# Kernel optimization log

Measured on AMD Instinct MI355X. Metric: run time of the kernel, lower is better.

The kernel has to match this reference:

```python
import jax, jax.numpy as jnp
import numpy as np

NUM_HEADS = 12


def setup_inputs() -> dict:
    key = jax.random.key(0)
    k1, k2, k3 = jax.random.split(key, 3)
    B, N, D = 8, 1024, 768
    x = jax.random.normal(k1, (B, N, D), dtype=jnp.float32)
    Wqkv = jax.random.normal(k2, (D, 3 * D), dtype=jnp.float32) * (D ** -0.5)
    Wproj = jax.random.normal(k3, (D, D), dtype=jnp.float32) * (D ** -0.5)
    bproj = jnp.zeros((D,), dtype=jnp.float32)
    return {"x": x, "Wqkv": Wqkv, "Wproj": Wproj, "bproj": bproj}


def reference(x, Wqkv, Wproj, bproj):
    B, N, D = x.shape
    H = NUM_HEADS
    d = D // H
    scale = d ** -0.5
    qkv = x @ Wqkv  # [B, N, 3D]; qkv_bias=False
    # 'b n (qkv h d) -> qkv b h n d'
    qkv = qkv.reshape(B, N, 3, H, d)
    q = jnp.transpose(qkv[:, :, 0], (0, 2, 1, 3))  # [B, H, N, d]
    k = jnp.transpose(qkv[:, :, 1], (0, 2, 1, 3))
    v = jnp.transpose(qkv[:, :, 2], (0, 2, 1, 3))
    attn = jnp.einsum('bhnd,bhmd->bhnm', q, k) * scale  # [B, H, N, N]
    attn = jax.nn.softmax(attn, axis=-1)
    out = jnp.einsum('bhnm,bhmd->bhnd', attn, v)  # [B, H, N, d]
    out = jnp.transpose(out, (0, 2, 1, 3)).reshape(B, N, D)  # 'b h n d -> b n (h d)'
    return out @ Wproj + bproj
```

## Files before the change

kernel.cpp:

```cpp
#include <hip/hip_runtime.h>
#include <math.h>
#include <stdint.h>

namespace {

constexpr int Nseq = 1024;
constexpr int Dm = 768;
constexpr int threeD = 2304;
constexpr int Mrows = 8192;
constexpr int Hh = 12;
constexpr float kScaleLog2 = 0.18033688011112042f;

using bf16x8 = __attribute__((ext_vector_type(8))) short;
using f32x4 = __attribute__((ext_vector_type(4))) float;
using f32x16 = __attribute__((ext_vector_type(16))) float;
using us4 = __attribute__((ext_vector_type(4))) unsigned short;

__device__ __forceinline__ unsigned short f2bf(float f) {
  union { float f; uint32_t u; } v;
  v.f = f;
  uint32_t r = v.u + 0x7fffu + ((v.u >> 16) & 1u);
  return (unsigned short)(r >> 16);
}

__device__ __forceinline__ float fexp2(float x) {
#if __has_builtin(__builtin_amdgcn_exp2f)
  return __builtin_amdgcn_exp2f(x);
#else
  float r;
  asm("v_exp_f32 %0, %1\n\ts_nop 0" : "=v"(r) : "v"(x));
  return r;
#endif
}

__device__ __forceinline__ uint32_t cvtpk_bf16(float lo, float hi) {
  uint32_t r;
  asm("v_cvt_pk_bf16_f32 %0, %1, %2" : "=v"(r) : "v"(lo), "v"(hi));
  return r;
}

__device__ __forceinline__ void gload_lds16(const void* g, void* l) {
  __builtin_amdgcn_global_load_lds(
      (const __attribute__((address_space(1))) unsigned int*)(uintptr_t)g,
      (__attribute__((address_space(3))) unsigned int*)(uintptr_t)l, 16, 0, 0);
}

__global__ __launch_bounds__(256) void cast_f32_bf16(
    const float* __restrict__ in, unsigned short* __restrict__ outp, int n4) {
  int i = blockIdx.x * blockDim.x + threadIdx.x;
  if (i < n4) {
    float4 v = ((const float4*)in)[i];
    us4 u = {f2bf(v.x), f2bf(v.y), f2bf(v.z), f2bf(v.w)};
    ((us4*)outp)[i] = u;
  }
}

__global__ __launch_bounds__(256) void transpose_cast(
    const float* __restrict__ W, unsigned short* __restrict__ Wt, int K, int N) {
  __shared__ unsigned short tile[32][33];
  const int n0 = blockIdx.x * 32, k0 = blockIdx.y * 32;
  const int tx = threadIdx.x & 31, ty = threadIdx.x >> 5;
#pragma unroll
  for (int i = 0; i < 32; i += 8)
    tile[ty + i][tx] = f2bf(W[(size_t)(k0 + ty + i) * N + n0 + tx]);
  __syncthreads();
#pragma unroll
  for (int i = 0; i < 32; i += 8)
    Wt[(size_t)(n0 + ty + i) * K + k0 + tx] = tile[tx][ty + i];
}

template <int MODE, int BM, int NCOLS>
__global__ __launch_bounds__(256) void gemm_bf16(
    const unsigned short* __restrict__ A, const unsigned short* __restrict__ Bt,
    void* __restrict__ C0, void* __restrict__ C1,
    const float* __restrict__ bias, int K) {
  constexpr int ASL = BM * 4;
  constexpr int TS = ASL + 512;
  constexpr int LPS = TS / 256;
  constexpr int MF = BM / 32;
  __shared__ unsigned short As[3][ASL * 8];
  __shared__ unsigned short Bs[3][512 * 8];
  const int tid = threadIdx.x;
  const int wid = tid >> 6;
  const int lane = tid & 63;
  const int l15 = lane & 15, lg = lane >> 4;
  const int p = blockIdx.x;
  const int cpx = gridDim.x >> 3;
  const int l = (p & 7) * cpx + (p >> 3);
  const int row0 = (l / NCOLS) * BM, col0 = (l % NCOLS) * 128;
  const int wr = (wid >> 1) * (BM / 2), wc = (wid & 1) * 64;

  auto stage = [&](int k0, int bufi) {
    unsigned short* as = As[bufi];
    unsigned short* bs = Bs[bufi];
#pragma unroll
    for (int it = 0; it < LPS; ++it) {
      const int s = it * 256 + tid;
      if (s < ASL) {
        const int r = s >> 2, c = s & 3;
        const int g = c ^ ((r >> 1) & 3);
        gload_lds16(&A[(size_t)(row0 + r) * K + k0 + g * 8],
                    &as[(s & ~63) * 8]);
      } else {
        const int s2 = s - ASL;
        const int r = s2 >> 2, c = s2 & 3;
        const int g = c ^ ((r >> 1) & 3);
        gload_lds16(&Bt[(size_t)(col0 + r) * K + k0 + g * 8],
                    &bs[(s2 & ~63) * 8]);
      }
    }
  };

  f32x4 acc[MF][4] = {};
  const int nt = K / 32;
  stage(0, 0);
  stage(32, 1);
  for (int t = 0; t < nt; ++t) {
    const int cur = t % 3;
    if (t + 2 < nt) {
      stage((t + 2) * 32, (t + 2) % 3);
      asm volatile("s_waitcnt vmcnt(%0)" ::"i"(2 * LPS) : "memory");
    } else if (t + 1 < nt) {
      asm volatile("s_waitcnt vmcnt(%0)" ::"i"(LPS) : "memory");
    } else {
      asm volatile("s_waitcnt vmcnt(0)" ::: "memory");
    }
    __builtin_amdgcn_s_barrier();
    bf16x8 av[MF], bv[4];
#pragma unroll
    for (int m = 0; m < MF; ++m) {
      const int ar = wr + m * 16 + l15;
      av[m] = *(const bf16x8*)&As[cur][(ar * 4 + (lg ^ ((ar >> 1) & 3))) * 8];
    }
#pragma unroll
    for (int n = 0; n < 4; ++n) {
      const int br = wc + n * 16 + l15;
      bv[n] = *(const bf16x8*)&Bs[cur][(br * 4 + (lg ^ ((br >> 1) & 3))) * 8];
    }
#pragma unroll
    for (int m = 0; m < MF; ++m)
#pragma unroll
      for (int n = 0; n < 4; ++n)
        acc[m][n] =
            __builtin_amdgcn_mfma_f32_16x16x32_bf16(av[m], bv[n], acc[m][n], 0, 0, 0);
    asm volatile("s_waitcnt lgkmcnt(0)" ::: "memory");
    __builtin_amdgcn_sched_barrier(0);
    __builtin_amdgcn_s_barrier();
  }
  if constexpr (MODE == 1) {
#pragma unroll
    for (int m = 0; m < MF; ++m)
#pragma unroll
      for (int n = 0; n < 4; ++n) {
        const int col = col0 + wc + n * 16 + l15;
#pragma unroll
        for (int rr = 0; rr < 4; ++rr)
          ((float*)C0)[(size_t)(row0 + wr + m * 16 + lg * 4 + rr) * Dm + col] =
              acc[m][n][rr] + bias[col];
      }
  } else if (col0 < 1536) {
#pragma unroll
    for (int m = 0; m < MF; ++m)
#pragma unroll
      for (int n = 0; n < 4; ++n) {
        const int col = col0 + wc + n * 16 + l15;
        const float qs = (col < 768) ? kScaleLog2 : 1.f;
#pragma unroll
        for (int rr = 0; rr < 4; ++rr)
          ((unsigned short*)C0)[(size_t)(row0 + wr + m * 16 + lg * 4 + rr) * 1536 +
                                col] = f2bf(acc[m][n][rr] * qs);
      }
  } else {
#pragma unroll
    for (int m = 0; m < MF; ++m)
#pragma unroll
      for (int n = 0; n < 4; ++n) {
        const int c = col0 + wc + n * 16 + l15 - 1536;
        const int row = row0 + wr + m * 16 + lg * 4;
        const int bb = row >> 10, n0 = row & 1023;
        us4 pk = {f2bf(acc[m][n][0]), f2bf(acc[m][n][1]), f2bf(acc[m][n][2]),
                  f2bf(acc[m][n][3])};
        *(us4*)&((unsigned short*)C1)[((size_t)bb * 768 + c) * 1024 + n0] = pk;
      }
  }
}

__global__ __launch_bounds__(256) void attn_mfma(
    const unsigned short* __restrict__ qkb, const unsigned short* __restrict__ vtb,
    unsigned short* __restrict__ outb) {
  constexpr int NT = Nseq / 64;
  __shared__ unsigned short Ks[3][64 * 64];
  __shared__ unsigned short Vs[3][64 * 64];
  const int tid = threadIdx.x;
  const int wid = tid >> 6, lane = tid & 63;
  const int l31 = lane & 31, hi = lane >> 5;
  const int p = blockIdx.x;
  const int l = (p & 7) * 96 + (p >> 3);
  const int qt = l & 7;
  const int hb = l >> 3;
  const int h = hb % Hh, b = hb / Hh;
  const size_t rb = (size_t)b * Nseq;
  const int hoff = h * 64;
  const size_t vbase = ((size_t)b * 768 + hoff) * 1024;

  const int qrow = qt * 128 + wid * 32 + l31;
  bf16x8 Qf[4];
#pragma unroll
  for (int ks = 0; ks < 4; ++ks)
    Qf[ks] = *(const bf16x8*)&qkb[(rb + qrow) * 1536 + hoff + ks * 16 + hi * 8];

  int strow[2], scol[2];
#pragma unroll
  for (int it = 0; it < 2; ++it) {
    const int ci = it * 256 + wid * 64 + lane;
    const int tr = ci >> 3, cc = ci & 7;
    strow[it] = tr;
    scol[it] = (cc ^ (tr & 7)) * 8;
  }

  auto stage = [&](int kt, int bufi) {
#pragma unroll
    for (int it = 0; it < 2; ++it) {
      const int ldsoff = (it * 256 + wid * 64) * 8;
      gload_lds16(&qkb[(rb + kt * 64 + strow[it]) * 1536 + 768 + hoff + scol[it]],
                  &Ks[bufi][ldsoff]);
      gload_lds16(&vtb[vbase + (size_t)strow[it] * 1024 + kt * 64 + scol[it]],
                  &Vs[bufi][ldsoff]);
    }
  };

  float l_run = 0.f;
  f32x16 o0 = {}, o1 = {};

  auto qk = [&](int bidx, f32x16& d0, f32x16& d1) {
    const unsigned short* ksb = Ks[bidx];
    d0 = {};
    d1 = {};
    __builtin_amdgcn_s_setprio(1);
#pragma unroll
    for (int ks = 0; ks < 4; ++ks) {
      const int c = 2 * ks + hi;
      {
        const int tr = l31;
        bf16x8 kf = *(const bf16x8*)&ksb[tr * 64 + ((c ^ (tr & 7)) * 8)];
        d0 = __builtin_amdgcn_mfma_f32_32x32x16_bf16(kf, Qf[ks], d0, 0, 0, 0);
      }
      {
        const int tr = l31 + 32;
        bf16x8 kf = *(const bf16x8*)&ksb[tr * 64 + ((c ^ (tr & 7)) * 8)];
        d1 = __builtin_amdgcn_mfma_f32_32x32x16_bf16(kf, Qf[ks], d1, 0, 0, 0);
      }
    }
    __builtin_amdgcn_s_setprio(0);
  };

  auto finish = [&](int bidx, f32x16& s0, f32x16& s1) {
#pragma unroll
    for (int i = 0; i < 16; ++i) {
      s0[i] = fexp2(s0[i]);
      s1[i] = fexp2(s1[i]);
    }
    float a[8];
#pragma unroll
    for (int i = 0; i < 8; ++i)
      a[i] = (s0[i] + s0[i + 8]) + (s1[i] + s1[i + 8]);
#pragma unroll
    for (int st = 4; st >= 1; st >>= 1)
#pragma unroll
      for (int i = 0; i < st; ++i) a[i] += a[i + st];
    l_run += a[0];
    bf16x8 Pf[4];
#pragma unroll
    for (int ks = 0; ks < 4; ++ks) {
      const f32x16 sv = (ks >> 1) ? s1 : s0;
      const int e0 = 8 * (ks & 1);
      uint32_t pe01 = cvtpk_bf16(sv[e0 + 0], sv[e0 + 1]);
      uint32_t pe23 = cvtpk_bf16(sv[e0 + 2], sv[e0 + 3]);
      uint32_t po01 = cvtpk_bf16(sv[e0 + 4], sv[e0 + 5]);
      uint32_t po23 = cvtpk_bf16(sv[e0 + 6], sv[e0 + 7]);
      asm("v_permlane32_swap_b32 %0, %1" : "+v"(pe01), "+v"(po01));
      asm("v_permlane32_swap_b32 %0, %1" : "+v"(pe23), "+v"(po23));
      union {
        uint32_t w[4];
        bf16x8 v;
      } u;
      u.w[0] = pe01;
      u.w[1] = pe23;
      u.w[2] = po01;
      u.w[3] = po23;
      Pf[ks] = u.v;
    }
    const unsigned short* vsb = Vs[bidx];
    __builtin_amdgcn_s_setprio(1);
#pragma unroll
    for (int ks = 0; ks < 4; ++ks) {
      const int c = 2 * ks + hi;
      {
        const int tr = l31;
        bf16x8 vf = *(const bf16x8*)&vsb[tr * 64 + ((c ^ (tr & 7)) * 8)];
        o0 = __builtin_amdgcn_mfma_f32_32x32x16_bf16(vf, Pf[ks], o0, 0, 0, 0);
      }
      {
        const int tr = l31 + 32;
        bf16x8 vf = *(const bf16x8*)&vsb[tr * 64 + ((c ^ (tr & 7)) * 8)];
        o1 = __builtin_amdgcn_mfma_f32_32x32x16_bf16(vf, Pf[ks], o1, 0, 0, 0);
      }
    }
    __builtin_amdgcn_s_setprio(0);
  };

  auto step = [&](int t, f32x16& c0, f32x16& c1, f32x16& n0, f32x16& n1) {
    if (t + 2 < NT) {
      stage(t + 2, (t + 2) % 3);
      asm volatile("s_waitcnt vmcnt(4)" ::: "memory");
    } else {
      asm volatile("s_waitcnt vmcnt(0)" ::: "memory");
    }
    __builtin_amdgcn_s_barrier();
    if (t + 1 < NT) qk((t + 1) % 3, n0, n1);
    finish(t % 3, c0, c1);
    asm volatile("s_waitcnt lgkmcnt(0)" ::: "memory");
    __builtin_amdgcn_sched_barrier(0);
    __builtin_amdgcn_s_barrier();
  };

  stage(0, 0);
  stage(1, 1);
  asm volatile("s_waitcnt vmcnt(4)" ::: "memory");
  __builtin_amdgcn_s_barrier();
  f32x16 sA0, sA1, sB0, sB1;
  qk(0, sA0, sA1);
  for (int t = 0; t < NT; t += 2) {
    step(t, sA0, sA1, sB0, sB1);
    step(t + 1, sB0, sB1, sA0, sA1);
  }
  const float lsum = l_run + __shfl_xor(l_run, 32);
  const float linv = 1.f / lsum;
  const size_t obase = (size_t)(rb + qrow) * Dm + hoff;
#pragma unroll
  for (int g = 0; g < 4; ++g) {
    us4 a4 = {f2bf(o0[g * 4 + 0] * linv), f2bf(o0[g * 4 + 1] * linv),
              f2bf(o0[g * 4 + 2] * linv), f2bf(o0[g * 4 + 3] * linv)};
    *(us4*)&outb[obase + g * 8 + hi * 4] = a4;
    us4 b4 = {f2bf(o1[g * 4 + 0] * linv), f2bf(o1[g * 4 + 1] * linv),
              f2bf(o1[g * 4 + 2] * linv), f2bf(o1[g * 4 + 3] * linv)};
    *(us4*)&outb[obase + 32 + g * 8 + hi * 4] = b4;
  }
}

}

extern "C" void kernel_launch(void* const* d_in, const int* in_sizes, int n_in,
                              void* d_out, int out_size, void* d_ws,
                              size_t ws_size, hipStream_t stream) {
  (void)in_sizes;
  (void)n_in;
  (void)out_size;
  (void)ws_size;
  const float* x = (const float*)d_in[0];
  const float* Wqkv = (const float*)d_in[1];
  const float* Wproj = (const float*)d_in[2];
  const float* bproj = (const float*)d_in[3];
  float* out = (float*)d_out;

  char* w = (char*)d_ws;
  unsigned short* xb = (unsigned short*)w;
  w += (size_t)Mrows * Dm * 2;
  unsigned short* wqkvt = (unsigned short*)w;
  w += (size_t)threeD * Dm * 2;
  unsigned short* wprojt = (unsigned short*)w;
  w += (size_t)Dm * Dm * 2;
  unsigned short* qkb = (unsigned short*)w;
  w += (size_t)Mrows * 1536 * 2;
  unsigned short* vtb = (unsigned short*)w;
  w += (size_t)96 * 64 * 1024 * 2;
  unsigned short* attnb = (unsigned short*)w;

  cast_f32_bf16<<<(Mrows * Dm / 4 + 255) / 256, 256, 0, stream>>>(
      x, xb, Mrows * Dm / 4);
  transpose_cast<<<dim3(threeD / 32, Dm / 32), 256, 0, stream>>>(
      Wqkv, wqkvt, Dm, threeD);
  transpose_cast<<<dim3(Dm / 32, Dm / 32), 256, 0, stream>>>(Wproj, wprojt, Dm, Dm);
  gemm_bf16<0, 128, 18><<<dim3(1152), 256, 0, stream>>>(
      xb, wqkvt, qkb, vtb, nullptr, Dm);
  attn_mfma<<<dim3(768), 256, 0, stream>>>(qkb, vtb, attnb);
  gemm_bf16<1, 64, 6><<<dim3(768), 256, 0, stream>>>(
      attnb, wprojt, out, nullptr, bproj, Dm);
}
```

Baseline: 120.1 us.

## Replace QKV GEMM with 256x256-tile 8-wave kernel using phased prefetch

```diff
diff --git a/kernel.cpp b/kernel.cpp
--- a/kernel.cpp
+++ b/kernel.cpp
@@ -69,11 +69,130 @@
     Wt[(size_t)(n0 + ty + i) * K + k0 + tx] = tile[tx][ty + i];
 }
 
-template <int MODE, int BM, int NCOLS>
-__global__ __launch_bounds__(256) void gemm_bf16(
+__global__ __launch_bounds__(512) void gemm256(
     const unsigned short* __restrict__ A, const unsigned short* __restrict__ Bt,
-    void* __restrict__ C0, void* __restrict__ C1,
-    const float* __restrict__ bias, int K) {
+    unsigned short* __restrict__ C0, unsigned short* __restrict__ C1, int Kdim) {
+  __shared__ unsigned short As[2][256 * 64];
+  __shared__ unsigned short Bs[2][256 * 64];
+  const int tid = threadIdx.x;
+  const int wid = tid >> 6, lane = tid & 63;
+  const int l15 = lane & 15, lg = lane >> 4;
+  const int xcd = blockIdx.x & 7, bi = blockIdx.x >> 3;
+  const int row0 = (xcd * 4 + (bi & 3)) * 256;
+  const int col0 = (bi >> 2) * 256;
+  const int wr = (wid >> 2) * 128, wc = (wid & 3) * 64;
+
+  auto stageA = [&](int kt, int b, int r) {
+    const int s = r * 512 + tid;
+    const int row = s >> 3, c = s & 7;
+    const int sc = c ^ (row & 7);
+    gload_lds16(&A[(size_t)(row0 + row) * Kdim + kt * 64 + sc * 8],
+                &As[b][(s & ~63) * 8]);
+  };
+  auto stageB = [&](int kt, int b, int r) {
+    const int s = r * 512 + tid;
+    const int row = s >> 3, c = s & 7;
+    const int sc = c ^ (row & 7);
+    gload_lds16(&Bt[(size_t)(col0 + row) * Kdim + kt * 64 + sc * 8],
+                &Bs[b][(s & ~63) * 8]);
+  };
+  auto rdA = [&](int b, int m, int ks) {
+    const int row = wr + m * 16 + l15;
+    const int sc = (ks * 4 + lg) ^ (row & 7);
+    return *(const bf16x8*)&As[b][(row * 8 + sc) * 8];
+  };
+  auto rdB = [&](int b, int n, int ks) {
+    const int row = wc + n * 16 + l15;
+    const int sc = (ks * 4 + lg) ^ (row & 7);
+    return *(const bf16x8*)&Bs[b][(row * 8 + sc) * 8];
+  };
+
+  f32x4 acc[8][4] = {};
+#pragma unroll
+  for (int r = 0; r < 4; ++r) stageA(0, 0, r);
+#pragma unroll
+  for (int r = 0; r < 4; ++r) stageB(0, 0, r);
+  asm volatile("s_waitcnt vmcnt(0)" ::: "memory");
+  __builtin_amdgcn_s_barrier();
+
+  const int NTK = Kdim / 64;
+  bf16x8 bfr[4][2], afr[2][2];
+
+#define GPHASE(MB, STAGE_BLOCK, TAIL_WAIT)                                     \
+  _Pragma("unroll") for (int mm = 0; mm < 2; ++mm)                             \
+      _Pragma("unroll") for (int ks = 0; ks < 2; ++ks) afr[mm][ks] =           \
+          rdA(cur, (MB) + mm, ks);                                             \
+  STAGE_BLOCK;                                                                 \
+  __builtin_amdgcn_s_barrier();                                                \
+  asm volatile("s_waitcnt lgkmcnt(0)" ::: "memory");                           \
+  __builtin_amdgcn_sched_barrier(0);                                           \
+  __builtin_amdgcn_s_setprio(1);                                               \
+  _Pragma("unroll") for (int mm = 0; mm < 2; ++mm)                             \
+      _Pragma("unroll") for (int n = 0; n < 4; ++n)                            \
+          _Pragma("unroll") for (int ks = 0; ks < 2; ++ks) acc[(MB) + mm][n] = \
+              __builtin_amdgcn_mfma_f32_16x16x32_bf16(afr[mm][ks], bfr[n][ks], \
+                                                      acc[(MB) + mm][n], 0, 0, \
+                                                      0);                      \
+  __builtin_amdgcn_s_setprio(0);                                               \
+  TAIL_WAIT;                                                                   \
+  __builtin_amdgcn_s_barrier();
+
+  for (int g = 0; g < NTK; ++g) {
+    const int cur = g & 1;
+    const int nb = cur ^ 1;
+    const bool pf = (g + 1 < NTK);
+#pragma unroll
+    for (int n = 0; n < 4; ++n)
+#pragma unroll
+      for (int ks = 0; ks < 2; ++ks) bfr[n][ks] = rdB(cur, n, ks);
+    GPHASE(0,
+           if (pf) {
+             stageA(g + 1, nb, 0);
+             stageA(g + 1, nb, 1);
+             stageB(g + 1, nb, 0);
+             stageB(g + 1, nb, 1);
+           },
+           )
+    GPHASE(2,
+           if (pf) {
+             stageA(g + 1, nb, 2);
+             stageA(g + 1, nb, 3);
+             stageB(g + 1, nb, 2);
+             stageB(g + 1, nb, 3);
+           },
+           )
+    GPHASE(4, , )
+    GPHASE(6, ,
+           asm volatile("s_waitcnt vmcnt(0)" ::: "memory");
+           __builtin_amdgcn_sched_barrier(0))
+  }
+#undef GPHASE
+
+#pragma unroll
+  for (int m = 0; m < 8; ++m)
+#pragma unroll
+    for (int n = 0; n < 4; ++n) {
+      const int col = col0 + wc + n * 16 + l15;
+      const int row = row0 + wr + m * 16 + lg * 4;
+      if (col < 1536) {
+        const float qs = (col < 768) ? kScaleLog2 : 1.f;
+#pragma unroll
+        for (int rr = 0; rr < 4; ++rr)
+          C0[(size_t)(row + rr) * 1536 + col] = f2bf(acc[m][n][rr] * qs);
+      } else {
+        const int c = col - 1536;
+        const int bb = row >> 10, n0 = row & 1023;
+        us4 pk = {f2bf(acc[m][n][0]), f2bf(acc[m][n][1]), f2bf(acc[m][n][2]),
+                  f2bf(acc[m][n][3])};
+        *(us4*)&C1[((size_t)bb * 768 + c) * 1024 + n0] = pk;
+      }
+    }
+}
+
+__global__ __launch_bounds__(256) void gemm_proj(
+    const unsigned short* __restrict__ A, const unsigned short* __restrict__ Bt,
+    float* __restrict__ C0, const float* __restrict__ bias, int K) {
+  constexpr int BM = 64, NCOLS = 6;
   constexpr int ASL = BM * 4;
   constexpr int TS = ASL + 512;
   constexpr int LPS = TS / 256;
@@ -99,8 +218,7 @@
       if (s < ASL) {
         const int r = s >> 2, c = s & 3;
         const int g = c ^ ((r >> 1) & 3);
-        gload_lds16(&A[(size_t)(row0 + r) * K + k0 + g * 8],
-                    &as[(s & ~63) * 8]);
+        gload_lds16(&A[(size_t)(row0 + r) * K + k0 + g * 8], &as[(s & ~63) * 8]);
       } else {
         const int s2 = s - ASL;
         const int r = s2 >> 2, c = s2 & 3;
@@ -147,42 +265,16 @@
     __builtin_amdgcn_sched_barrier(0);
     __builtin_amdgcn_s_barrier();
   }
-  if constexpr (MODE == 1) {
-#pragma unroll
-    for (int m = 0; m < MF; ++m)
-#pragma unroll
-      for (int n = 0; n < 4; ++n) {
-        const int col = col0 + wc + n * 16 + l15;
-#pragma unroll
-        for (int rr = 0; rr < 4; ++rr)
-          ((float*)C0)[(size_t)(row0 + wr + m * 16 + lg * 4 + rr) * Dm + col] =
-              acc[m][n][rr] + bias[col];
-      }
-  } else if (col0 < 1536) {
-#pragma unroll
-    for (int m = 0; m < MF; ++m)
-#pragma unroll
-      for (int n = 0; n < 4; ++n) {
-        const int col = col0 + wc + n * 16 + l15;
-        const float qs = (col < 768) ? kScaleLog2 : 1.f;
-#pragma unroll
-        for (int rr = 0; rr < 4; ++rr)
-          ((unsigned short*)C0)[(size_t)(row0 + wr + m * 16 + lg * 4 + rr) * 1536 +
-                                col] = f2bf(acc[m][n][rr] * qs);
-      }
-  } else {
-#pragma unroll
-    for (int m = 0; m < MF; ++m)
-#pragma unroll
-      for (int n = 0; n < 4; ++n) {
-        const int c = col0 + wc + n * 16 + l15 - 1536;
-        const int row = row0 + wr + m * 16 + lg * 4;
-        const int bb = row >> 10, n0 = row & 1023;
-        us4 pk = {f2bf(acc[m][n][0]), f2bf(acc[m][n][1]), f2bf(acc[m][n][2]),
-                  f2bf(acc[m][n][3])};
-        *(us4*)&((unsigned short*)C1)[((size_t)bb * 768 + c) * 1024 + n0] = pk;
-      }
-  }
+#pragma unroll
+  for (int m = 0; m < MF; ++m)
+#pragma unroll
+    for (int n = 0; n < 4; ++n) {
+      const int col = col0 + wc + n * 16 + l15;
+#pragma unroll
+      for (int rr = 0; rr < 4; ++rr)
+        C0[(size_t)(row0 + wr + m * 16 + lg * 4 + rr) * Dm + col] =
+            acc[m][n][rr] + bias[col];
+    }
 }
 
 __global__ __launch_bounds__(256) void attn_mfma(
@@ -381,9 +473,7 @@
   transpose_cast<<<dim3(threeD / 32, Dm / 32), 256, 0, stream>>>(
       Wqkv, wqkvt, Dm, threeD);
   transpose_cast<<<dim3(Dm / 32, Dm / 32), 256, 0, stream>>>(Wproj, wprojt, Dm, Dm);
-  gemm_bf16<0, 128, 18><<<dim3(1152), 256, 0, stream>>>(
-      xb, wqkvt, qkb, vtb, nullptr, Dm);
+  gemm256<<<dim3(288), 512, 0, stream>>>(xb, wqkvt, qkb, vtb, Dm);
   attn_mfma<<<dim3(768), 256, 0, stream>>>(qkb, vtb, attnb);
-  gemm_bf16<1, 64, 6><<<dim3(768), 256, 0, stream>>>(
-      attnb, wprojt, out, nullptr, bproj, Dm);
-}
+  gemm_proj<<<dim3(768), 256, 0, stream>>>(attnb, wprojt, out, bproj, Dm);
+}
```

Measured after the change: 129.0 us. 7.3% more time.
